# Kernel optimization log

Hardware: AMD Instinct MI355X
Metric: run time of the kernel (lower is better)

## Reference

```python
import jax, jax.numpy as jnp
import numpy as np

N, E, D, H = 100000, 1000000, 128, 8
DH = D // H
SCALE = 1.0 / np.sqrt(DH)


def setup_inputs() -> dict:
    key = jax.random.key(0)
    ks = jax.random.split(key, 12)
    inp = {
        "x": jax.random.normal(ks[0], (N, D), jnp.float32),
        "edge_index": jax.random.randint(ks[1], (2, E), 0, N, dtype=jnp.int64),
        "a": jnp.array(0.25, jnp.float32),  # shared PReLU slope
    }
    names = ["Wq1", "Wk1", "Wv1", "Ws1", "Wq2", "Wk2", "Wv2", "Ws2"]
    for i, n in enumerate(names):
        # kaiming_normal_: std = sqrt(2 / fan_in)
        inp[n] = jax.random.normal(ks[2 + i], (D, D), jnp.float32) * np.sqrt(2.0 / D)
        inp["b" + n[1:]] = jnp.zeros((D,), jnp.float32)
    return inp


def prelu(x, a):
    return jnp.where(x >= 0, x, a * x)


def transformer_conv(x, src, dst, Wq, bq, Wk, bk, Wv, bv, Ws, bs):
    # PyG TransformerConv: query from target (dst), key/value from source (src),
    # scatter-softmax over incoming edges of each dst node, root skip via lin_skip.
    q = (x @ Wq + bq).reshape(N, H, DH)
    k = (x @ Wk + bk).reshape(N, H, DH)
    v = (x @ Wv + bv).reshape(N, H, DH)
    score = jnp.einsum("ehd,ehd->eh", q[dst], k[src]) * SCALE  # [E, H]
    m = jax.lax.stop_gradient(jax.ops.segment_max(score, dst, num_segments=N))  # [N, H]
    e = jnp.exp(score - m[dst])
    s = jax.ops.segment_sum(e, dst, num_segments=N)  # [N, H]
    alpha = e / s[dst]  # scatter-softmax, [E, H]
    agg = jax.ops.segment_sum(alpha[..., None] * v[src], dst, num_segments=N)  # [N, H, DH]
    return agg.reshape(N, D) + x @ Ws + bs


def reference(x, edge_index, a,
              Wq1, bq1, Wk1, bk1, Wv1, bv1, Ws1, bs1,
              Wq2, bq2, Wk2, bk2, Wv2, bv2, Ws2, bs2):
    src, dst = edge_index[0], edge_index[1]
    h = transformer_conv(x, src, dst, Wq1, bq1, Wk1, bk1, Wv1, bv1, Ws1, bs1)
    h = prelu(h, a)
    h = transformer_conv(h, src, dst, Wq2, bq2, Wk2, bk2, Wv2, bv2, Ws2, bs2)
    h = h + x
    return prelu(h, a)
```

## Files before the change

### kernel.cpp

```cpp
#include <hip/hip_runtime.h>
#include <hip/hip_bf16.h>
#include <math.h>

#define D 128
#define SCALE 0.25f
#define NEG_BIG (-1e30f)
#define SLOTS 32

#define BN 256
#define NBMAX 512
#define CAP 7936
#define P1B 256

typedef __attribute__((ext_vector_type(8))) short bf16x8;
typedef __attribute__((ext_vector_type(4))) float f32x4;
typedef __attribute__((ext_vector_type(2))) float f32x2;

__device__ inline __hip_bfloat162 pack2(float a, float b) {
    __hip_bfloat162 h;
    h.x = __float2bfloat16(a);
    h.y = __float2bfloat16(b);
    return h;
}

__device__ inline int detect_is64(const int* __restrict__ ei) {
    int lane = threadIdx.x & 63;
    int v = ei[2 * lane + 1];
    unsigned long long b = __ballot(v != 0);
    return b == 0ULL;
}

struct PackArgs { const float* w[8]; };

__global__ __launch_bounds__(256) void prep_phase1(
    PackArgs pa, __hip_bfloat16* __restrict__ WtP,
    const float* __restrict__ x, __hip_bfloat16* __restrict__ xb, int n4,
    const int* __restrict__ ei, int E, int NB,
    int* __restrict__ gcount, unsigned long long* __restrict__ bucketbuf)
{
    __shared__ int hist[NBMAX];
    __shared__ int lbase[NBMAX];
    __shared__ int lcur[NBMAX];

    int b = blockIdx.x;
    int tid = threadIdx.x;
    if (b < 8) {
        const float* W = pa.w[b];
        __hip_bfloat16* dst = WtP + (size_t)b * 128 * 128;
        for (int idx = tid; idx < 128 * 128; idx += 256) {
            int c = idx & 127, k = idx >> 7;
            dst[(size_t)c * 128 + k] = __float2bfloat16(W[(size_t)k * 128 + c]);
        }
        return;
    }
    if (b < 8 + P1B) {
        int blk = b - 8;
        int is64 = detect_is64(ei);
        int slice = (E + P1B - 1) / P1B;
        int base = blk * slice;
        int lim = base + slice; if (lim > E) lim = E;

        for (int i = tid; i < NB; i += 256) { hist[i] = 0; lcur[i] = 0; }
        __syncthreads();

        for (int e = base + tid; e < lim; e += 256) {
            int d = is64 ? ei[2 * E + 2 * e] : ei[E + e];
            atomicAdd(&hist[d >> 8], 1);
        }
        __syncthreads();

        for (int i = tid; i < NB; i += 256) {
            int h = hist[i];
            lbase[i] = h ? atomicAdd(&gcount[i], h) : 0;
        }
        __syncthreads();

        for (int e = base + tid; e < lim; e += 256) {
            int s = is64 ? ei[2 * e]         : ei[e];
            int d = is64 ? ei[2 * E + 2 * e] : ei[E + e];
            int bb = d >> 8;
            int pos = lbase[bb] + atomicAdd(&lcur[bb], 1);
            if (pos < CAP)
                bucketbuf[(size_t)bb * CAP + pos] =
                    ((unsigned long long)(unsigned)d << 32) | (unsigned)s;
        }
        return;
    }
    {
        int i = (b - 8 - P1B) * 256 + tid;
        if (i < n4) {
            float4 v = ((const float4*)x)[i];
            ((__hip_bfloat162*)xb)[2 * i]     = pack2(v.x, v.y);
            ((__hip_bfloat162*)xb)[2 * i + 1] = pack2(v.z, v.w);
        }
    }
}

#define TSTR 136

__device__ __forceinline__ void gemm_body(
    int bx, __hip_bfloat16* bufA, __hip_bfloat16* bufB,
    const __hip_bfloat16* __restrict__ A, const __hip_bfloat16* __restrict__ Wt,
    const float* __restrict__ bq, const float* __restrict__ bk,
    const float* __restrict__ bv, const float* __restrict__ bs,
    __hip_bfloat16* __restrict__ qb, __hip_bfloat16* __restrict__ kv,
    __hip_bfloat16* __restrict__ skipb, int M)
{
    const int tid = threadIdx.x;
    const int w = tid >> 6, lane = tid & 63;
    const int wr = w >> 1, wc = w & 1;
    const int blk0 = bx * 64;
    const int rowBase = blk0 + wr * 32;
    const int l16 = lane & 15;
    const int quad = lane >> 4;

    bf16x8 xfrag[2][4];
    #pragma unroll
    for (int i = 0; i < 2; ++i) {
        int r = rowBase + i * 16 + l16;
        if (r >= M) r = M - 1;
        #pragma unroll
        for (int kb = 0; kb < 4; ++kb)
            xfrag[i][kb] = *(const bf16x8*)(A + (size_t)r * D + kb * 32 + quad * 8);
    }

    const float* biases[4] = {bq, bk, bv, bs};

    for (int cb = 0; cb < 4; ++cb) {
        const __hip_bfloat16* Wblk = Wt + (size_t)cb * 128 * 128;
        f32x4 acc[2][4];
        #pragma unroll
        for (int i = 0; i < 2; i++)
            #pragma unroll
            for (int jt = 0; jt < 4; jt++) acc[i][jt] = (f32x4){0.f, 0.f, 0.f, 0.f};

        #pragma unroll
        for (int kb = 0; kb < 4; ++kb) {
            const int k0 = kb * 32 + quad * 8;
            #pragma unroll
            for (int jt = 0; jt < 4; ++jt) {
                int c = wc * 64 + jt * 16 + l16;
                bf16x8 wfrag = *(const bf16x8*)(Wblk + (size_t)c * D + k0);
                acc[0][jt] = __builtin_amdgcn_mfma_f32_16x16x32_bf16(wfrag, xfrag[0][kb], acc[0][jt], 0, 0, 0);
                acc[1][jt] = __builtin_amdgcn_mfma_f32_16x16x32_bf16(wfrag, xfrag[1][kb], acc[1][jt], 0, 0, 0);
            }
        }

        __hip_bfloat16* dst = (cb == 2) ? bufB : bufA;
        const float* bias = biases[cb];
        #pragma unroll
        for (int jt = 0; jt < 4; ++jt) {
            int c0 = wc * 64 + jt * 16 + quad * 4;
            float4 bb = *(const float4*)(bias + c0);
            #pragma unroll
            for (int i = 0; i < 2; ++i) {
                int lrow = wr * 32 + i * 16 + l16;
                f32x4 vv = acc[i][jt];
                __hip_bfloat162 h0 = pack2(vv[0] + bb.x, vv[1] + bb.y);
                __hip_bfloat162 h1 = pack2(vv[2] + bb.z, vv[3] + bb.w);
                float2 st; st.x = *(float*)&h0; st.y = *(float*)&h1;
                *(float2*)(&dst[lrow * TSTR + c0]) = st;
            }
        }

        if (cb == 1) continue;

        __syncthreads();

        if (cb == 0 || cb == 3) {
            __hip_bfloat16* gout = (cb == 0) ? qb : skipb;
            #pragma unroll
            for (int it = 0; it < 4; ++it) {
                int lrow = it * 16 + (tid >> 4);
                int grow = blk0 + lrow;
                if (grow < M) {
                    float4 vv = *(const float4*)(&bufA[lrow * TSTR + (tid & 15) * 8]);
                    *(float4*)(gout + (size_t)grow * D + (tid & 15) * 8) = vv;
                }
            }
        } else {
            #pragma unroll
            for (int it = 0; it < 8; ++it) {
                int lrow = it * 8 + (tid >> 5);
                int grow = blk0 + lrow;
                int g = tid & 31;
                if (grow < M) {
                    float2 kk = *(const float2*)(&bufA[lrow * TSTR + g * 4]);
                    float2 vv = *(const float2*)(&bufB[lrow * TSTR + g * 4]);
                    float4 o; o.x = kk.x; o.y = kk.y; o.z = vv.x; o.w = vv.y;
                    *(float4*)(kv + (size_t)grow * 256 + g * 8) = o;
                }
            }
        }
        __syncthreads();
    }
}

__global__ __launch_bounds__(256) void gemm_mfma(
    const __hip_bfloat16* __restrict__ A, const __hip_bfloat16* __restrict__ Wt,
    const float* __restrict__ bq, const float* __restrict__ bk,
    const float* __restrict__ bv, const float* __restrict__ bs,
    __hip_bfloat16* __restrict__ qb, __hip_bfloat16* __restrict__ kv,
    __hip_bfloat16* __restrict__ skipb, int M)
{
    __shared__ __hip_bfloat16 smem[2 * 64 * TSTR];
    gemm_body(blockIdx.x, smem, smem + 64 * TSTR, A, Wt, bq, bk, bv, bs, qb, kv, skipb, M);
}

__global__ __launch_bounds__(256) void csr_gemm1(
    const __hip_bfloat16* __restrict__ A, const __hip_bfloat16* __restrict__ Wt,
    const float* __restrict__ bq, const float* __restrict__ bk,
    const float* __restrict__ bv, const float* __restrict__ bs,
    __hip_bfloat16* __restrict__ qb, __hip_bfloat16* __restrict__ kv,
    __hip_bfloat16* __restrict__ skipb, int M,
    const int* __restrict__ gcount, const unsigned long long* __restrict__ bucketbuf,
    int NB,
    int* __restrict__ deg, int* __restrict__ slots,
    unsigned long long* __restrict__ ovf, int* __restrict__ ovfcnt)
{
    __shared__ __hip_bfloat16 smem[2 * 64 * TSTR];
    const int bx = blockIdx.x;
    const int tid = threadIdx.x;

    if (bx < NB) {
        int* ldeg  = (int*)smem;
        int* lslot = ldeg + BN;

        int cnt = gcount[bx]; if (cnt > CAP) cnt = CAP;
        ldeg[tid] = 0;
        __syncthreads();

        const unsigned long long* bb = bucketbuf + (size_t)bx * CAP;
        for (int i = tid; i < cnt; i += 256) {
            unsigned long long e = bb[i];
            int d = (int)(e >> 32);
            int s = (int)(e & 0xffffffffULL);
            int ln = d & (BN - 1);
            int pos = atomicAdd(&ldeg[ln], 1);
            if (pos < SLOTS) {
                lslot[ln * SLOTS + pos] = s;
            } else {
                int op = atomicAdd(ovfcnt, 1);
                ovf[op] = e;
            }
        }
        __syncthreads();

        int n0 = bx << 8;
        if (n0 + tid < M) deg[n0 + tid] = ldeg[tid];
        for (int i = tid; i < BN * SLOTS / 4; i += 256) {
            int node = n0 + (i >> 3);
            if (node < M)
                ((int4*)slots)[(size_t)n0 * 8 + i] = ((int4*)lslot)[i];
        }
        __syncthreads();
    }

    gemm_body(bx, smem, smem + 64 * TSTR, A, Wt, bq, bk, bv, bs, qb, kv, skipb, M);
}

__device__ inline void store4(float* base, size_t off, float o0, float o1, float o2, float o3) {
    f32x4 v; v[0] = o0; v[1] = o1; v[2] = o2; v[3] = o3;
    __builtin_nontemporal_store(v, (f32x4*)(base + off));
}
__device__ inline void store4(__hip_bfloat16* base, size_t off, float o0, float o1, float o2, float o3) {
    __hip_bfloat162 h0 = pack2(o0, o1), h1 = pack2(o2, o3);
    float2 st; st.x = *(float*)&h0; st.y = *(float*)&h1;
    *(float2*)(base + off) = st;
}

template <typename OutT>
__global__ __launch_bounds__(256) void attn_agg(
    const __hip_bfloat16* __restrict__ qb, const __hip_bfloat16* __restrict__ kv,
    const int* __restrict__ deg, const int* __restrict__ slots,
    const unsigned long long* __restrict__ ovf, const int* __restrict__ ovfcnt,
    const __hip_bfloat16* __restrict__ skip, const __hip_bfloat16* __restrict__ residb,
    const float* __restrict__ a_ptr, OutT* __restrict__ out, int Nn) {
    int tid = threadIdx.x;
    int lane = tid & 63;
    int half = lane >> 5;
    int lh = lane & 31;
    int n = blockIdx.x * 8 + (tid >> 6) * 2 + half;
    bool valid = (n < Nn);
    int nc = valid ? n : (Nn - 1);
    const float a = a_ptr[0];

    int myslot = __builtin_nontemporal_load(slots + nc * SLOTS + lh);
    myslot = ((unsigned)myslot < (unsigned)Nn) ? myslot : 0;

    f32x2 qraw = __builtin_nontemporal_load((const f32x2*)(qb + (size_t)nc * D + 4 * lh));
    float qx = qraw[0], qy = qraw[1];
    __hip_bfloat162 q01 = *(__hip_bfloat162*)&qx;
    __hip_bfloat162 q23 = *(__hip_bfloat162*)&qy;
    float q0 = __bfloat162float(q01.x) * SCALE, q1 = __bfloat162float(q01.y) * SCALE;
    float q2 = __bfloat162float(q23.x) * SCALE, q3 = __bfloat162float(q23.y) * SCALE;

    float s = 0.f, A0 = 0.f, A1 = 0.f, A2 = 0.f, A3 = 0.f;

    int cnt = valid ? __builtin_nontemporal_load(deg + nc) : 0;
    int cmain = min(cnt, SLOTS);
    int cmax = max(cmain, __shfl_xor(cmain, 32));

    const float4* kvp4 = (const float4*)kv;

    for (int t = 0; t < cmax; t += 8) {
        float4 f[8];
        float sc[8];
        #pragma unroll
        for (int i = 0; i < 8; ++i) {
            int sval = __shfl(myslot, half * 32 + t + i);
            int src = (t + i < cmain) ? sval : 0;
            f[i] = kvp4[(size_t)src * 32 + lh];
        }
        #pragma unroll
        for (int i = 0; i < 8; ++i) {
            __hip_bfloat162 k01 = *(__hip_bfloat162*)&f[i].x;
            __hip_bfloat162 k23 = *(__hip_bfloat162*)&f[i].y;
            float p = q0 * __bfloat162float(k01.x) + q1 * __bfloat162float(k01.y)
                    + q2 * __bfloat162float(k23.x) + q3 * __bfloat162float(k23.y);
            p += __shfl_xor(p, 1);
            p += __shfl_xor(p, 2);
            sc[i] = (t + i < cmain) ? p : NEG_BIG;
        }
        #pragma unroll
        for (int i = 0; i < 8; ++i) {
            float wgt = __expf(sc[i]);
            __hip_bfloat162 v01 = *(__hip_bfloat162*)&f[i].z;
            __hip_bfloat162 v23 = *(__hip_bfloat162*)&f[i].w;
            A0 += wgt * __bfloat162float(v01.x);
            A1 += wgt * __bfloat162float(v01.y);
            A2 += wgt * __bfloat162float(v23.x);
            A3 += wgt * __bfloat162float(v23.y);
            s += wgt;
        }
    }

    if (__any(cnt > SLOTS)) {
        int oc = *ovfcnt;
        for (int i = 0; i < oc; ++i) {
            unsigned long long e = ovf[i];
            int dd = (int)(e >> 32);
            int ss = (int)(e & 0xffffffffULL);
            bool take = (dd == nc) && (cnt > SLOTS) && valid;
            ss = ((unsigned)ss < (unsigned)Nn) ? ss : 0;
            float4 fo = kvp4[(size_t)ss * 32 + lh];
            __hip_bfloat162 k01 = *(__hip_bfloat162*)&fo.x;
            __hip_bfloat162 k23 = *(__hip_bfloat162*)&fo.y;
            float p = q0 * __bfloat162float(k01.x) + q1 * __bfloat162float(k01.y)
                    + q2 * __bfloat162float(k23.x) + q3 * __bfloat162float(k23.y);
            p += __shfl_xor(p, 1);
            p += __shfl_xor(p, 2);
            float wgt = take ? __expf(p) : 0.f;
            __hip_bfloat162 v01 = *(__hip_bfloat162*)&fo.z;
            __hip_bfloat162 v23 = *(__hip_bfloat162*)&fo.w;
            A0 += wgt * __bfloat162float(v01.x);
            A1 += wgt * __bfloat162float(v01.y);
            A2 += wgt * __bfloat162float(v23.x);
            A3 += wgt * __bfloat162float(v23.y);
            s += wgt;
        }
    }

    if (!valid) return;
    float inv = (cnt > 0) ? 1.f / s : 0.f;
    f32x2 skr = __builtin_nontemporal_load((const f32x2*)(skip + (size_t)n * D + 4 * lh));
    float skx = skr[0], sky = skr[1];
    __hip_bfloat162 s01 = *(__hip_bfloat162*)&skx;
    __hip_bfloat162 s23 = *(__hip_bfloat162*)&sky;
    float o0 = A0 * inv + __bfloat162float(s01.x);
    float o1 = A1 * inv + __bfloat162float(s01.y);
    float o2 = A2 * inv + __bfloat162float(s23.x);
    float o3 = A3 * inv + __bfloat162float(s23.y);
    if (residb) {
        f32x2 rr = __builtin_nontemporal_load((const f32x2*)(residb + (size_t)n * D + 4 * lh));
        float rx = rr[0], ry = rr[1];
        __hip_bfloat162 r01 = *(__hip_bfloat162*)&rx;
        __hip_bfloat162 r23 = *(__hip_bfloat162*)&ry;
        o0 += __bfloat162float(r01.x);
        o1 += __bfloat162float(r01.y);
        o2 += __bfloat162float(r23.x);
        o3 += __bfloat162float(r23.y);
    }
    o0 = (o0 >= 0.f) ? o0 : a * o0;
    o1 = (o1 >= 0.f) ? o1 : a * o1;
    o2 = (o2 >= 0.f) ? o2 : a * o2;
    o3 = (o3 >= 0.f) ? o3 : a * o3;
    store4(out, (size_t)n * D + 4 * lh, o0, o1, o2, o3);
}

extern "C" void kernel_launch(void* const* d_in, const int* in_sizes, int n_in,
                              void* d_out, int out_size, void* d_ws, size_t ws_size,
                              hipStream_t stream) {
    const float* x  = (const float*)d_in[0];
    const int*   ei = (const int*)d_in[1];
    const float* a  = (const float*)d_in[2];
    const float* Wq1 = (const float*)d_in[3];  const float* bq1 = (const float*)d_in[4];
    const float* Wk1 = (const float*)d_in[5];  const float* bk1 = (const float*)d_in[6];
    const float* Wv1 = (const float*)d_in[7];  const float* bv1 = (const float*)d_in[8];
    const float* Ws1 = (const float*)d_in[9];  const float* bs1 = (const float*)d_in[10];
    const float* Wq2 = (const float*)d_in[11]; const float* bq2 = (const float*)d_in[12];
    const float* Wk2 = (const float*)d_in[13]; const float* bk2 = (const float*)d_in[14];
    const float* Wv2 = (const float*)d_in[15]; const float* bv2 = (const float*)d_in[16];
    const float* Ws2 = (const float*)d_in[17]; const float* bs2 = (const float*)d_in[18];

    const int N = in_sizes[0] / D;
    const int E = in_sizes[1] / 2;
    const size_t NF = (size_t)N * D;
    const int NB = (N + BN - 1) / BN;

    char* wp = (char*)d_ws;
    __hip_bfloat16* xb    = (__hip_bfloat16*)wp; wp += NF * 2;
    __hip_bfloat16* h1b   = (__hip_bfloat16*)wp; wp += NF * 2;
    __hip_bfloat16* qb    = (__hip_bfloat16*)wp; wp += NF * 2;
    __hip_bfloat16* kv    = (__hip_bfloat16*)wp; wp += NF * 4;
    __hip_bfloat16* skipb = (__hip_bfloat16*)wp; wp += NF * 2;
    __hip_bfloat16* WtP   = (__hip_bfloat16*)wp; wp += 2 * 512 * 128 * 2;
    int* deg    = (int*)wp;                wp += (size_t)N * 4;
    int* ovfcnt = (int*)wp;                wp += 64;
    int* gcount = (int*)wp;                wp += NBMAX * 4;
    size_t zbytes = 64 + NBMAX * 4;
    int* slots  = (int*)wp;                wp += (size_t)N * SLOTS * 4;
    unsigned long long* ovf = (unsigned long long*)wp; wp += (size_t)E * 8;
    unsigned long long* bucketbuf = (unsigned long long*)h1b;
    float* out = (float*)d_out;

    const int TB = 256;
    int gGemm = (N + 63) / 64;
    int gAttn = (N + 7) / 8;
    int n4 = (int)(NF / 4);
    int gCvt = (n4 + TB - 1) / TB;

    PackArgs pa;
    pa.w[0] = Wq1; pa.w[1] = Wk1; pa.w[2] = Wv1; pa.w[3] = Ws1;
    pa.w[4] = Wq2; pa.w[5] = Wk2; pa.w[6] = Wv2; pa.w[7] = Ws2;

    (void)hipMemsetAsync(ovfcnt, 0, zbytes, stream);

    hipLaunchKernelGGL(prep_phase1, dim3(8 + P1B + gCvt), dim3(TB), 0, stream,
                       pa, WtP, x, xb, n4, ei, E, NB, gcount, bucketbuf);

    hipLaunchKernelGGL(csr_gemm1, dim3(gGemm), dim3(TB), 0, stream,
                       xb, WtP, bq1, bk1, bv1, bs1, qb, kv, skipb, N,
                       gcount, bucketbuf, NB, deg, slots, ovf, ovfcnt);
    hipLaunchKernelGGL(attn_agg<__hip_bfloat16>, dim3(gAttn), dim3(TB), 0, stream,
                       qb, kv, deg, slots, ovf, ovfcnt, skipb,
                       (const __hip_bfloat16*)nullptr, a, h1b, N);

    hipLaunchKernelGGL(gemm_mfma, dim3(gGemm), dim3(TB), 0, stream,
                       h1b, WtP + 512 * 128, bq2, bk2, bv2, bs2, qb, kv, skipb, N);
    hipLaunchKernelGGL(attn_agg<float>, dim3(gAttn), dim3(TB), 0, stream,
                       qb, kv, deg, slots, ovf, ovfcnt, skipb, xb, a, out, N);
}
```

Measured before the change: 464.0 us.

## Fuse layer-1 attention aggregation into layer-2 GEMM via shared-memory staging

Adds a kernel where each block first computes layer-1 attention outputs for its 64 rows, applying PReLU and packing to bf16 in LDS. It then runs the layer-2 QKV/skip GEMM directly from LDS instead of re-reading h1 from global memory. This removes the h1 write/read round trip and one kernel launch. Layer-2 K/V go to a separate workspace buffer, because other blocks still gather layer-1 K/V from neighbours. The trade-off is that the latency-bound gather now runs in fewer blocks that loop serially over 8 row groups, with occupancy limited by the GEMM's register and LDS footprint.

After: 483.6 us. 1.04x slower.

```diff
diff --git a/kernel.cpp b/kernel.cpp
--- a/kernel.cpp
+++ b/kernel.cpp
@@ -98,9 +98,10 @@
 
 #define TSTR 136
 
+template <bool ALDS>
 __device__ __forceinline__ void gemm_body(
     int bx, __hip_bfloat16* bufA, __hip_bfloat16* bufB,
-    const __hip_bfloat16* __restrict__ A, const __hip_bfloat16* __restrict__ Wt,
+    const __hip_bfloat16* A, const __hip_bfloat16* __restrict__ Wt,
     const float* __restrict__ bq, const float* __restrict__ bk,
     const float* __restrict__ bv, const float* __restrict__ bs,
     __hip_bfloat16* __restrict__ qb, __hip_bfloat16* __restrict__ kv,
@@ -117,12 +118,20 @@
     bf16x8 xfrag[2][4];
     #pragma unroll
     for (int i = 0; i < 2; ++i) {
-        int r = rowBase + i * 16 + l16;
-        if (r >= M) r = M - 1;
-        #pragma unroll
-        for (int kb = 0; kb < 4; ++kb)
-            xfrag[i][kb] = *(const bf16x8*)(A + (size_t)r * D + kb * 32 + quad * 8);
-    }
+        if (ALDS) {
+            int lr = wr * 32 + i * 16 + l16;
+            #pragma unroll
+            for (int kb = 0; kb < 4; ++kb)
+                xfrag[i][kb] = *(const bf16x8*)(A + lr * TSTR + kb * 32 + quad * 8);
+        } else {
+            int r = rowBase + i * 16 + l16;
+            if (r >= M) r = M - 1;
+            #pragma unroll
+            for (int kb = 0; kb < 4; ++kb)
+                xfrag[i][kb] = *(const bf16x8*)(A + (size_t)r * D + kb * 32 + quad * 8);
+        }
+    }
+    if (ALDS) __syncthreads();
 
     const float* biases[4] = {bq, bk, bv, bs};
 
@@ -204,7 +213,7 @@
     __hip_bfloat16* __restrict__ skipb, int M)
 {
     __shared__ __hip_bfloat16 smem[2 * 64 * TSTR];
-    gemm_body(blockIdx.x, smem, smem + 64 * TSTR, A, Wt, bq, bk, bv, bs, qb, kv, skipb, M);
+    gemm_body<false>(blockIdx.x, smem, smem + 64 * TSTR, A, Wt, bq, bk, bv, bs, qb, kv, skipb, M);
 }
 
 __global__ __launch_bounds__(256) void csr_gemm1(
@@ -256,35 +265,16 @@
         __syncthreads();
     }
 
-    gemm_body(bx, smem, smem + 64 * TSTR, A, Wt, bq, bk, bv, bs, qb, kv, skipb, M);
-}
-
-__device__ inline void store4(float* base, size_t off, float o0, float o1, float o2, float o3) {
-    f32x4 v; v[0] = o0; v[1] = o1; v[2] = o2; v[3] = o3;
-    __builtin_nontemporal_store(v, (f32x4*)(base + off));
-}
-__device__ inline void store4(__hip_bfloat16* base, size_t off, float o0, float o1, float o2, float o3) {
-    __hip_bfloat162 h0 = pack2(o0, o1), h1 = pack2(o2, o3);
-    float2 st; st.x = *(float*)&h0; st.y = *(float*)&h1;
-    *(float2*)(base + off) = st;
-}
-
-template <typename OutT>
-__global__ __launch_bounds__(256) void attn_agg(
-    const __hip_bfloat16* __restrict__ qb, const __hip_bfloat16* __restrict__ kv,
+    gemm_body<false>(bx, smem, smem + 64 * TSTR, A, Wt, bq, bk, bv, bs, qb, kv, skipb, M);
+}
+
+__device__ __forceinline__ float4 attn_core(
+    const __hip_bfloat16* qb, const float4* kvp4,
     const int* __restrict__ deg, const int* __restrict__ slots,
     const unsigned long long* __restrict__ ovf, const int* __restrict__ ovfcnt,
-    const __hip_bfloat16* __restrict__ skip, const __hip_bfloat16* __restrict__ residb,
-    const float* __restrict__ a_ptr, OutT* __restrict__ out, int Nn) {
-    int tid = threadIdx.x;
-    int lane = tid & 63;
-    int half = lane >> 5;
-    int lh = lane & 31;
-    int n = blockIdx.x * 8 + (tid >> 6) * 2 + half;
-    bool valid = (n < Nn);
-    int nc = valid ? n : (Nn - 1);
-    const float a = a_ptr[0];
-
+    const __hip_bfloat16* skip, const __hip_bfloat16* __restrict__ residb,
+    float a, int nc, bool valid, int half, int lh, int Nn)
+{
     int myslot = __builtin_nontemporal_load(slots + nc * SLOTS + lh);
     myslot = ((unsigned)myslot < (unsigned)Nn) ? myslot : 0;
 
@@ -300,8 +290,6 @@
     int cnt = valid ? __builtin_nontemporal_load(deg + nc) : 0;
     int cmain = min(cnt, SLOTS);
     int cmax = max(cmain, __shfl_xor(cmain, 32));
-
-    const float4* kvp4 = (const float4*)kv;
 
     for (int t = 0; t < cmax; t += 8) {
         float4 f[8];
@@ -361,9 +349,8 @@
         }
     }
 
-    if (!valid) return;
     float inv = (cnt > 0) ? 1.f / s : 0.f;
-    f32x2 skr = __builtin_nontemporal_load((const f32x2*)(skip + (size_t)n * D + 4 * lh));
+    f32x2 skr = __builtin_nontemporal_load((const f32x2*)(skip + (size_t)nc * D + 4 * lh));
     float skx = skr[0], sky = skr[1];
     __hip_bfloat162 s01 = *(__hip_bfloat162*)&skx;
     __hip_bfloat162 s23 = *(__hip_bfloat162*)&sky;
@@ -372,7 +359,7 @@
     float o2 = A2 * inv + __bfloat162float(s23.x);
     float o3 = A3 * inv + __bfloat162float(s23.y);
     if (residb) {
-        f32x2 rr = __builtin_nontemporal_load((const f32x2*)(residb + (size_t)n * D + 4 * lh));
+        f32x2 rr = __builtin_nontemporal_load((const f32x2*)(residb + (size_t)nc * D + 4 * lh));
         float rx = rr[0], ry = rr[1];
         __hip_bfloat162 r01 = *(__hip_bfloat162*)&rx;
         __hip_bfloat162 r23 = *(__hip_bfloat162*)&ry;
@@ -385,7 +372,81 @@
     o1 = (o1 >= 0.f) ? o1 : a * o1;
     o2 = (o2 >= 0.f) ? o2 : a * o2;
     o3 = (o3 >= 0.f) ? o3 : a * o3;
-    store4(out, (size_t)n * D + 4 * lh, o0, o1, o2, o3);
+    return make_float4(o0, o1, o2, o3);
+}
+
+__device__ inline void store4(float* base, size_t off, float o0, float o1, float o2, float o3) {
+    f32x4 v; v[0] = o0; v[1] = o1; v[2] = o2; v[3] = o3;
+    __builtin_nontemporal_store(v, (f32x4*)(base + off));
+}
+__device__ inline void store4(__hip_bfloat16* base, size_t off, float o0, float o1, float o2, float o3) {
+    __hip_bfloat162 h0 = pack2(o0, o1), h1 = pack2(o2, o3);
+    float2 st; st.x = *(float*)&h0; st.y = *(float*)&h1;
+    *(float2*)(base + off) = st;
+}
+
+template <typename OutT>
+__global__ __launch_bounds__(256) void attn_agg(
+    const __hip_bfloat16* __restrict__ qb, const __hip_bfloat16* __restrict__ kv,
+    const int* __restrict__ deg, const int* __restrict__ slots,
+    const unsigned long long* __restrict__ ovf, const int* __restrict__ ovfcnt,
+    const __hip_bfloat16* __restrict__ skip, const __hip_bfloat16* __restrict__ residb,
+    const float* __restrict__ a_ptr, OutT* __restrict__ out, int Nn) {
+    int tid = threadIdx.x;
+    int lane = tid & 63;
+    int half = lane >> 5;
+    int lh = lane & 31;
+    int n = blockIdx.x * 8 + (tid >> 6) * 2 + half;
+    bool valid = (n < Nn);
+    int nc = valid ? n : (Nn - 1);
+    const float a = a_ptr[0];
+    const float4* kvp4 = (const float4*)kv;
+
+    float4 o = attn_core(qb, kvp4, deg, slots, ovf, ovfcnt, skip, residb,
+                         a, nc, valid, half, lh, Nn);
+    if (!valid) return;
+    store4(out, (size_t)n * D + 4 * lh, o.x, o.y, o.z, o.w);
+}
+
+__global__ __launch_bounds__(256) void attn1_gemm2(
+    const __hip_bfloat16* qb, const __hip_bfloat16* __restrict__ kv1,
+    const int* __restrict__ deg, const int* __restrict__ slots,
+    const unsigned long long* __restrict__ ovf, const int* __restrict__ ovfcnt,
+    const __hip_bfloat16* skipb, const float* __restrict__ a_ptr,
+    const __hip_bfloat16* __restrict__ Wt2,
+    const float* __restrict__ bq2, const float* __restrict__ bk2,
+    const float* __restrict__ bv2, const float* __restrict__ bs2,
+    __hip_bfloat16* qb_out, __hip_bfloat16* __restrict__ kv2,
+    __hip_bfloat16* skipb_out, int M)
+{
+    __shared__ __hip_bfloat16 smem[2 * 64 * TSTR];
+    __hip_bfloat16* bufA = smem;
+    __hip_bfloat16* bufB = smem + 64 * TSTR;
+
+    const int tid = threadIdx.x;
+    const int lane = tid & 63;
+    const int half = lane >> 5;
+    const int lh = lane & 31;
+    const int blk0 = blockIdx.x * 64;
+    const float a = a_ptr[0];
+    const float4* kvp4 = (const float4*)kv1;
+
+    for (int p = 0; p < 8; ++p) {
+        int lrow = p * 8 + (tid >> 6) * 2 + half;
+        int n = blk0 + lrow;
+        bool valid = (n < M);
+        int nc = valid ? n : (M - 1);
+        float4 o = attn_core(qb, kvp4, deg, slots, ovf, ovfcnt, skipb,
+                             (const __hip_bfloat16*)nullptr,
+                             a, nc, valid, half, lh, M);
+        __hip_bfloat162 h0 = pack2(o.x, o.y), h1 = pack2(o.z, o.w);
+        float2 st; st.x = *(float*)&h0; st.y = *(float*)&h1;
+        *(float2*)(&bufA[lrow * TSTR + 4 * lh]) = st;
+    }
+    __syncthreads();
+
+    gemm_body<true>(blockIdx.x, bufA, bufB, bufA, Wt2, bq2, bk2, bv2, bs2,
+                    qb_out, kv2, skipb_out, M);
 }
 
 extern "C" void kernel_launch(void* const* d_in, const int* in_sizes, int n_in,
@@ -421,6 +482,8 @@
     size_t zbytes = 64 + NBMAX * 4;
     int* slots  = (int*)wp;                wp += (size_t)N * SLOTS * 4;
     unsigned long long* ovf = (unsigned long long*)wp; wp += (size_t)E * 8;
+    __hip_bfloat16* kv2 = (__hip_bfloat16*)wp; wp += NF * 4;
+    size_t need_fused = (size_t)(wp - (char*)d_ws);
     unsigned long long* bucketbuf = (unsigned long long*)h1b;
     float* out = (float*)d_out;
 
@@ -442,12 +505,21 @@
     hipLaunchKernelGGL(csr_gemm1, dim3(gGemm), dim3(TB), 0, stream,
                        xb, WtP, bq1, bk1, bv1, bs1, qb, kv, skipb, N,
                        gcount, bucketbuf, NB, deg, slots, ovf, ovfcnt);
-    hipLaunchKernelGGL(attn_agg<__hip_bfloat16>, dim3(gAttn), dim3(TB), 0, stream,
-                       qb, kv, deg, slots, ovf, ovfcnt, skipb,
-                       (const __hip_bfloat16*)nullptr, a, h1b, N);
-
-    hipLaunchKernelGGL(gemm_mfma, dim3(gGemm), dim3(TB), 0, stream,
-                       h1b, WtP + 512 * 128, bq2, bk2, bv2, bs2, qb, kv, skipb, N);
-    hipLaunchKernelGGL(attn_agg<float>, dim3(gAttn), dim3(TB), 0, stream,
-                       qb, kv, deg, slots, ovf, ovfcnt, skipb, xb, a, out, N);
-}
+
+    if (ws_size >= need_fused) {
+        hipLaunchKernelGGL(attn1_gemm2, dim3(gGemm), dim3(TB), 0, stream,
+                           qb, kv, deg, slots, ovf, ovfcnt, skipb, a,
+                           WtP + 512 * 128, bq2, bk2, bv2, bs2,
+                           qb, kv2, skipb, N);
+        hipLaunchKernelGGL(attn_agg<float>, dim3(gAttn), dim3(TB), 0, stream,
+                           qb, kv2, deg, slots, ovf, ovfcnt, skipb, xb, a, out, N);
+    } else {
+        hipLaunchKernelGGL(attn_agg<__hip_bfloat16>, dim3(gAttn), dim3(TB), 0, stream,
+                           qb, kv, deg, slots, ovf, ovfcnt, skipb,
+                           (const __hip_bfloat16*)nullptr, a, h1b, N);
+        hipLaunchKernelGGL(gemm_mfma, dim3(gGemm), dim3(TB), 0, stream,
+                           h1b, WtP + 512 * 128, bq2, bk2, bv2, bs2, qb, kv, skipb, N);
+        hipLaunchKernelGGL(attn_agg<float>, dim3(gAttn), dim3(TB), 0, stream,
+                           qb, kv, deg, slots, ovf, ovfcnt, skipb, xb, a, out, N);
+    }
+}
```
